# Kernel optimization log

Measured on AMD Instinct MI355X. Metric: run time of the kernel, lower is better.

The kernel has to match this reference:

```python
import jax, jax.numpy as jnp
import numpy as np

B, T, C, H = 4, 2048, 1024, 16
HD = C // H  # head dim = 64


def _rope(x, pos):
    """Rotary embedding. x: [B,H,T,hd], pos: [B,T] int positions."""
    half = x.shape[-1] // 2
    inv_freq = 1.0 / (10000.0 ** (jnp.arange(half, dtype=jnp.float32) / half))
    ang = pos.astype(jnp.float32)[:, None, :, None] * inv_freq  # [B,1,T,half]
    cos, sin = jnp.cos(ang), jnp.sin(ang)
    x1, x2 = x[..., :half], x[..., half:]
    return jnp.concatenate([x1 * cos - x2 * sin, x1 * sin + x2 * cos], axis=-1)


def setup_inputs() -> dict:
    key = jax.random.key(0)
    k1, k2, k3 = jax.random.split(key, 3)
    x = jax.random.normal(k1, (B, T, C), dtype=jnp.float32)
    W_attn = jax.random.normal(k2, (C, 3 * C), dtype=jnp.float32) * (1.0 / np.sqrt(C))
    W_proj = jax.random.normal(k3, (C, C), dtype=jnp.float32) * (1.0 / np.sqrt(C))
    indices = jnp.broadcast_to(jnp.arange(T, dtype=jnp.int32)[None, :], (B, T))
    return {"x": x, "W_attn": W_attn, "W_proj": W_proj, "indices": indices}


def reference(x, W_attn, W_proj, indices):
    # QKV projection (bias=False)
    qkv = x @ W_attn  # [B,T,3C]
    q, k, v = jnp.split(qkv, 3, axis=-1)

    def to_heads(t):
        return t.reshape(B, T, H, HD).transpose(0, 2, 1, 3)  # [B,H,T,hd]

    q, k, v = to_heads(q), to_heads(k), to_heads(v)
    # RoPE on q and k at positions given by indices (pos_emb_closure.adapt_*)
    q = _rope(q, indices)
    k = _rope(k, indices)

    # attn_mask = k_indices <= q_indices, shape [B,1,T,T]
    mask = indices[:, None, None, :] <= indices[:, None, :, None]

    att = jnp.einsum("bhqd,bhkd->bhqk", q, k) * (1.0 / np.sqrt(HD))
    att = jnp.where(mask, att, jnp.float32(-jnp.inf))
    att = jax.nn.softmax(att, axis=-1)
    y = jnp.einsum("bhqk,bhkd->bhqd", att, v)  # [B,H,T,hd]
    y = y.transpose(0, 2, 1, 3).reshape(B, T, C)
    return y @ W_proj
```

## Files before the change

### kernel.cpp

```cpp
#include <hip/hip_runtime.h>
#include <math.h>

namespace {
constexpr int Bsz = 4;
constexpr int T   = 2048;
constexpr int C   = 1024;
constexpr int H   = 16;
constexpr int HD  = 64;

typedef short bf16x8 __attribute__((ext_vector_type(8)));
typedef float f32x4  __attribute__((ext_vector_type(4)));
typedef unsigned int u32x4 __attribute__((ext_vector_type(4)));

#if defined(__has_builtin)
#if __has_builtin(__builtin_amdgcn_global_load_lds)
#define HAVE_GLL 1
typedef __attribute__((address_space(3))) unsigned int lds_u32_t;
typedef __attribute__((address_space(1))) unsigned int g_u32_t;
#define GLL16(gp, lp)                                                        \
  __builtin_amdgcn_global_load_lds((const g_u32_t*)(gp), (lds_u32_t*)(lp),   \
                                   16, 0, 0)
#endif
#endif

__device__ __forceinline__ unsigned short f2bf(float f) {
  unsigned int u = __builtin_bit_cast(unsigned int, f);
  u += 0x7FFFu + ((u >> 16) & 1u);
  return (unsigned short)(u >> 16);
}
__device__ __forceinline__ float bf2f(unsigned short s) {
  unsigned int u = ((unsigned int)s) << 16;
  return __builtin_bit_cast(float, u);
}
__device__ __forceinline__ unsigned int cvtpk_bf16(float a, float b) {
  unsigned int r;
  asm("v_cvt_pk_bf16_f32 %0, %1, %2" : "=v"(r) : "v"(a), "v"(b));
  return r;
}

__global__ __launch_bounds__(256) void f32_to_bf16_kernel(
    const float* __restrict__ in, unsigned short* __restrict__ out, int n4) {
  int i = blockIdx.x * 256 + threadIdx.x;
  if (i < n4) {
    float4 v = ((const float4*)in)[i];
    ushort4 o;
    o.x = f2bf(v.x); o.y = f2bf(v.y); o.z = f2bf(v.z); o.w = f2bf(v.w);
    ((ushort4*)out)[i] = o;
  }
}

__global__ __launch_bounds__(256) void transpose_bf16_kernel(
    const float* __restrict__ W, unsigned short* __restrict__ Wt, int K, int N) {
  __shared__ float tile[32][33];
  const int n0 = blockIdx.x * 32, k0 = blockIdx.y * 32;
  const int r = threadIdx.x >> 3, c4 = threadIdx.x & 7;
  float4 v = *(const float4*)(W + (size_t)(k0 + r) * N + n0 + c4 * 4);
  tile[r][c4 * 4 + 0] = v.x;
  tile[r][c4 * 4 + 1] = v.y;
  tile[r][c4 * 4 + 2] = v.z;
  tile[r][c4 * 4 + 3] = v.w;
  __syncthreads();
  ushort4 o;
  o.x = f2bf(tile[c4 * 4 + 0][r]);
  o.y = f2bf(tile[c4 * 4 + 1][r]);
  o.z = f2bf(tile[c4 * 4 + 2][r]);
  o.w = f2bf(tile[c4 * 4 + 3][r]);
  *(ushort4*)(Wt + (size_t)(n0 + r) * K + k0 + c4 * 4) = o;
}

template <int MODE>
__global__ __launch_bounds__(256) void gemm_bt(
    const unsigned short* __restrict__ A, const unsigned short* __restrict__ Bt,
    float* __restrict__ Cout, unsigned short* __restrict__ qp,
    unsigned short* __restrict__ kp, unsigned short* __restrict__ vp,
    int M, int N, int K) {
  __shared__ __align__(16) unsigned short As[128 * 32];
  __shared__ __align__(16) unsigned short Bs[128 * 32];
  const int tid = threadIdx.x;
  const int lane = tid & 63, w = tid >> 6;
  const int wr = w & 1, wc = w >> 1;
  const int l15 = lane & 15, quad = lane >> 4;
  const int m0 = blockIdx.y * 128, n0 = blockIdx.x * 128;

  const int srow = lane >> 2;
  const int schunk = (lane & 3) * 8;
  const unsigned short* gA = A + (size_t)(m0 + w * 32 + srow) * K + schunk;
  const unsigned short* gB = Bt + (size_t)(n0 + w * 32 + srow) * K + schunk;
  unsigned short* lA0 = &As[(w * 32) * 32 + lane * 8];
  unsigned short* lA1 = &As[(w * 32 + 16) * 32 + lane * 8];
  unsigned short* lB0 = &Bs[(w * 32) * 32 + lane * 8];
  unsigned short* lB1 = &Bs[(w * 32 + 16) * 32 + lane * 8];

  f32x4 acc[4][4] = {};

  for (int k0 = 0; k0 < K; k0 += 32) {
    __syncthreads();
#ifdef HAVE_GLL
    GLL16(gA + k0, lA0);
    GLL16(gA + (size_t)16 * K + k0, lA1);
    GLL16(gB + k0, lB0);
    GLL16(gB + (size_t)16 * K + k0, lB1);
#else
    *(uint4*)lA0 = *(const uint4*)(gA + k0);
    *(uint4*)lA1 = *(const uint4*)(gA + (size_t)16 * K + k0);
    *(uint4*)lB0 = *(const uint4*)(gB + k0);
    *(uint4*)lB1 = *(const uint4*)(gB + (size_t)16 * K + k0);
#endif
    __syncthreads();

    bf16x8 af[4], bfr[4];
#pragma unroll
    for (int mf = 0; mf < 4; ++mf)
      af[mf] = *(const bf16x8*)&As[(wr * 64 + mf * 16 + l15) * 32 + quad * 8];
#pragma unroll
    for (int nf = 0; nf < 4; ++nf)
      bfr[nf] = *(const bf16x8*)&Bs[(wc * 64 + nf * 16 + l15) * 32 + quad * 8];
#pragma unroll
    for (int mf = 0; mf < 4; ++mf)
#pragma unroll
      for (int nf = 0; nf < 4; ++nf)
        acc[mf][nf] = __builtin_amdgcn_mfma_f32_16x16x32_bf16(
            af[mf], bfr[nf], acc[mf][nf], 0, 0, 0);
  }

#pragma unroll
  for (int mf = 0; mf < 4; ++mf) {
    const int row0 = m0 + wr * 64 + mf * 16 + quad * 4;
#pragma unroll
    for (int nf = 0; nf < 4; ++nf) {
      if (MODE == 0) {
#pragma unroll
        for (int r = 0; r < 4; ++r) {
          const int col = n0 + wc * 64 + nf * 16 + l15;
          Cout[(size_t)(row0 + r) * N + col] = acc[mf][nf][r];
        }
      } else {
        const int col = n0 + wc * 64 + nf * 16 + l15;
        const int which = col >> 10;
        const int rem = col & (C - 1);
        const int h = rem >> 6, hd = rem & 63;
        const int b = row0 >> 11, t0 = row0 & (T - 1);
        if (which == 2) {
          ushort4 pv;
          pv.x = f2bf(acc[mf][nf][0]);
          pv.y = f2bf(acc[mf][nf][1]);
          pv.z = f2bf(acc[mf][nf][2]);
          pv.w = f2bf(acc[mf][nf][3]);
          *(ushort4*)(vp + (((size_t)(b * H + h)) * HD + hd) * T + t0) = pv;
        } else {
          unsigned short* dst = which == 0 ? qp : kp;
#pragma unroll
          for (int r = 0; r < 4; ++r)
            dst[(((size_t)(b * H + h)) * T + t0 + r) * HD + hd] =
                f2bf(acc[mf][nf][r]);
        }
      }
    }
  }
}

__global__ __launch_bounds__(256) void rope_bf16(unsigned short* __restrict__ q,
                                                 unsigned short* __restrict__ k,
                                                 const int* __restrict__ idx) {
  const int g = blockIdx.x * 8 + (threadIdx.x >> 5);
  const int lane = threadIdx.x & 31;
  const int b = g >> 11, t = g & (T - 1);
  const int pos = idx[b * T + t];
  const float inv = exp2f((float)lane * -0.41524101186f);
  float sn, cs;
  sincosf((float)pos * inv, &sn, &cs);
  const float SC = 0.18033688f;
  const float snq = sn * SC, csq = cs * SC;
  const size_t base0 = ((size_t)b * H * T + t) * HD + lane;
#pragma unroll 4
  for (int h = 0; h < H; ++h) {
    const size_t base = base0 + (size_t)h * T * HD;
    float x1 = bf2f(q[base]), x2 = bf2f(q[base + 32]);
    q[base]      = f2bf(x1 * csq - x2 * snq);
    q[base + 32] = f2bf(x1 * snq + x2 * csq);
    x1 = bf2f(k[base]);
    x2 = bf2f(k[base + 32]);
    k[base]      = f2bf(x1 * cs - x2 * sn);
    k[base + 32] = f2bf(x1 * sn + x2 * cs);
  }
}

__global__ __launch_bounds__(256) void flash_attn_mfma(
    const unsigned short* __restrict__ q, const unsigned short* __restrict__ k,
    const unsigned short* __restrict__ vt, const int* __restrict__ idx,
    unsigned short* __restrict__ y) {
  __shared__ __align__(16) unsigned short Ks[2][64 * 64];
  __shared__ __align__(16) unsigned short Vts[2][64 * 64];

  const int tid = threadIdx.x;
  const int lane = tid & 63, w = tid >> 6;
  const int l15 = lane & 15, quad = lane >> 4;

  const int flat = (blockIdx.z * H + blockIdx.y) * 16 + blockIdx.x;
  const int slot_ = flat >> 3;
  const int bh_i = (flat & 7) * 8 + (slot_ >> 4);
  const int bx = slot_ & 15;
  const int h = bh_i & (H - 1), b = bh_i >> 4;

  const size_t bh = (size_t)bh_i;
  const unsigned short* qg = q + bh * T * HD;
  const unsigned short* kg = k + bh * T * HD;
  const unsigned short* vg = vt + bh * HD * T;
  const int* idxb = idx + b * T;

  int km;
  {
    const int4* p4 = (const int4*)(idxb + (lane << 5));
    int4 v0 = p4[0];
    int m = max(max(v0.x, v0.y), max(v0.z, v0.w));
#pragma unroll
    for (int j = 1; j < 8; ++j) {
      int4 v = p4[j];
      m = max(m, max(max(v.x, v.y), max(v.z, v.w)));
    }
    km = max(m, __shfl_xor(m, 1));
  }

  const int r1 = tid >> 3, c1 = tid & 7;
  const int r2 = r1 + 32;
  const int xr1 = (r1 & 7) << 3;
  const int swS1 = r1 * 64 + ((c1 * 8) ^ xr1);
  const int swS2 = r2 * 64 + ((c1 * 8) ^ xr1);
  const int vbase = 32 * (c1 >> 2) + 16 * (c1 & 1) + 4 * ((c1 >> 1) & 1);
  const int vo1a = r1 * 64 + ((vbase + 0) ^ xr1);
  const int vo1b = r1 * 64 + ((vbase + 8) ^ xr1);
  const int vo2a = r2 * 64 + ((vbase + 0) ^ xr1);
  const int vo2b = r2 * 64 + ((vbase + 8) ^ xr1);
  const int rx = (l15 & 7) << 3;

  for (int ti = 0; ti < 2; ++ti) {
    const int qt = (ti == 0) ? bx : 31 - bx;
    const int qrow = qt * 64 + w * 16 + l15;

    const bf16x8 bq0 = *(const bf16x8*)(qg + (size_t)qrow * HD + quad * 8);
    const bf16x8 bq1 = *(const bf16x8*)(qg + (size_t)qrow * HD + 32 + quad * 8);
    const int pq = idxb[qrow];
    int mq = pq;
    mq = min(mq, __shfl_xor(mq, 1));
    mq = min(mq, __shfl_xor(mq, 2));
    mq = min(mq, __shfl_xor(mq, 4));
    mq = min(mq, __shfl_xor(mq, 8));
    const unsigned long long bal = __ballot(km > mq);

    float m_run = -1e38f, lq = 0.0f;
    f32x4 Oa[4] = {};

    {
      uint4 ka = *(const uint4*)(kg + (size_t)r1 * HD + c1 * 8);
      uint4 kb = *(const uint4*)(kg + (size_t)r2 * HD + c1 * 8);
      uint4 va = *(const uint4*)(vg + (size_t)r1 * T + c1 * 8);
      uint4 vb = *(const uint4*)(vg + (size_t)r2 * T + c1 * 8);
      __syncthreads();
      *(uint4*)&Ks[0][swS1] = ka;
      *(uint4*)&Ks[0][swS2] = kb;
      *(uint2*)&Vts[0][vo1a] = make_uint2(va.x, va.y);
      *(uint2*)&Vts[0][vo1b] = make_uint2(va.z, va.w);
      *(uint2*)&Vts[0][vo2a] = make_uint2(vb.x, vb.y);
      *(uint2*)&Vts[0][vo2b] = make_uint2(vb.z, vb.w);
    }

    for (int kt = 0; kt <= qt; ++kt) {
      const int cur = kt & 1;
      const int k0 = kt * 64;
      __syncthreads();

      uint4 nka, nkb, nva, nvb;
      if (kt < qt) {
        const int kn = k0 + 64;
        nka = *(const uint4*)(kg + (size_t)(kn + r1) * HD + c1 * 8);
        nkb = *(const uint4*)(kg + (size_t)(kn + r2) * HD + c1 * 8);
        nva = *(const uint4*)(vg + (size_t)r1 * T + kn + c1 * 8);
        nvb = *(const uint4*)(vg + (size_t)r2 * T + kn + c1 * 8);
      }

      f32x4 Sa[4];
      __builtin_amdgcn_s_setprio(1);
#pragma unroll
      for (int nf = 0; nf < 4; ++nf) {
        const int row = (nf * 16 + l15) * 64;
        bf16x8 ak0 = *(const bf16x8*)&Ks[cur][row + ((quad * 8) ^ rx)];
        bf16x8 ak1 = *(const bf16x8*)&Ks[cur][row + ((32 + quad * 8) ^ rx)];
        f32x4 s = {};
        s = __builtin_amdgcn_mfma_f32_16x16x32_bf16(ak0, bq0, s, 0, 0, 0);
        s = __builtin_amdgcn_mfma_f32_16x16x32_bf16(ak1, bq1, s, 0, 0, 0);
        Sa[nf] = s;
      }
      __builtin_amdgcn_s_setprio(0);

      if ((bal >> (kt + kt)) & 1ull) {
#pragma unroll
        for (int nf = 0; nf < 4; ++nf) {
          const int4 pk4 = *(const int4*)(idxb + k0 + nf * 16 + quad * 4);
          if (pk4.x > pq) Sa[nf][0] = -3e38f;
          if (pk4.y > pq) Sa[nf][1] = -3e38f;
          if (pk4.z > pq) Sa[nf][2] = -3e38f;
          if (pk4.w > pq) Sa[nf][3] = -3e38f;
        }
      }

      float mx = fmaxf(
          fmaxf(fmaxf(fmaxf(Sa[0][0], Sa[0][1]), Sa[0][2]),
                fmaxf(fmaxf(Sa[0][3], Sa[1][0]), Sa[1][1])),
          fmaxf(fmaxf(fmaxf(Sa[1][2], Sa[1][3]), Sa[2][0]),
                fmaxf(fmaxf(Sa[2][1], Sa[2][2]), Sa[2][3])));
      mx = fmaxf(mx, fmaxf(fmaxf(Sa[3][0], Sa[3][1]), fmaxf(Sa[3][2], Sa[3][3])));
      mx = fmaxf(mx, __shfl_xor(mx, 16));
      mx = fmaxf(mx, __shfl_xor(mx, 32));

      if (!__all(mx <= m_run + 8.0f)) {
        const float mn = fmaxf(m_run, mx);
        const float alpha = exp2f(m_run - mn);
        m_run = mn;
        lq *= alpha;
#pragma unroll
        for (int nfd = 0; nfd < 4; ++nfd)
#pragma unroll
          for (int r = 0; r < 4; ++r) Oa[nfd][r] *= alpha;
      }

      u32x4 w0, w1;
#pragma unroll
      for (int nf = 0; nf < 4; ++nf) {
        float p0 = exp2f(Sa[nf][0] - m_run);
        float p1 = exp2f(Sa[nf][1] - m_run);
        float p2 = exp2f(Sa[nf][2] - m_run);
        float p3 = exp2f(Sa[nf][3] - m_run);
        Sa[nf][0] = p0; Sa[nf][1] = p1; Sa[nf][2] = p2; Sa[nf][3] = p3;
        if (nf < 2) {
          w0[nf * 2 + 0] = cvtpk_bf16(p0, p1);
          w0[nf * 2 + 1] = cvtpk_bf16(p2, p3);
        } else {
          w1[(nf - 2) * 2 + 0] = cvtpk_bf16(p0, p1);
          w1[(nf - 2) * 2 + 1] = cvtpk_bf16(p2, p3);
        }
      }
      const bf16x8 bp0 = __builtin_bit_cast(bf16x8, w0);
      const bf16x8 bp1 = __builtin_bit_cast(bf16x8, w1);

      __builtin_amdgcn_s_setprio(1);
#pragma unroll
      for (int nfd = 0; nfd < 4; ++nfd) {
        const int vrow = (nfd * 16 + l15) * 64;
        bf16x8 av0 = *(const bf16x8*)&Vts[cur][vrow + ((quad * 8) ^ rx)];
        bf16x8 av1 = *(const bf16x8*)&Vts[cur][vrow + ((32 + quad * 8) ^ rx)];
        Oa[nfd] = __builtin_amdgcn_mfma_f32_16x16x32_bf16(av0, bp0, Oa[nfd], 0, 0, 0);
        Oa[nfd] = __builtin_amdgcn_mfma_f32_16x16x32_bf16(av1, bp1, Oa[nfd], 0, 0, 0);
      }
      __builtin_amdgcn_s_setprio(0);

      lq += ((Sa[0][0] + Sa[0][1]) + (Sa[0][2] + Sa[0][3])) +
            ((Sa[1][0] + Sa[1][1]) + (Sa[1][2] + Sa[1][3])) +
            ((Sa[2][0] + Sa[2][1]) + (Sa[2][2] + Sa[2][3])) +
            ((Sa[3][0] + Sa[3][1]) + (Sa[3][2] + Sa[3][3]));

      if (kt < qt) {
        const int nxt = cur ^ 1;
        *(uint4*)&Ks[nxt][swS1] = nka;
        *(uint4*)&Ks[nxt][swS2] = nkb;
        *(uint2*)&Vts[nxt][vo1a] = make_uint2(nva.x, nva.y);
        *(uint2*)&Vts[nxt][vo1b] = make_uint2(nva.z, nva.w);
        *(uint2*)&Vts[nxt][vo2a] = make_uint2(nvb.x, nvb.y);
        *(uint2*)&Vts[nxt][vo2b] = make_uint2(nvb.z, nvb.w);
      }
    }

    float lsum = lq;
    lsum += __shfl_xor(lsum, 16);
    lsum += __shfl_xor(lsum, 32);
    const float rl = 1.0f / lsum;
    const size_t base = ((size_t)b * T + qrow) * (size_t)C + h * HD;
#pragma unroll
    for (int nfd = 0; nfd < 4; ++nfd) {
      ushort4 o;
      o.x = f2bf(Oa[nfd][0] * rl);
      o.y = f2bf(Oa[nfd][1] * rl);
      o.z = f2bf(Oa[nfd][2] * rl);
      o.w = f2bf(Oa[nfd][3] * rl);
      *(ushort4*)(y + base + nfd * 16 + quad * 4) = o;
    }
  }
}

}

extern "C" void kernel_launch(void* const* d_in, const int* in_sizes, int n_in,
                              void* d_out, int out_size, void* d_ws,
                              size_t ws_size, hipStream_t stream) {
  const float* x      = (const float*)d_in[0];
  const float* W_attn = (const float*)d_in[1];
  const float* W_proj = (const float*)d_in[2];
  const int* indices  = (const int*)d_in[3];
  float* out = (float*)d_out;

  const size_t nM = (size_t)Bsz * T * C;
  unsigned short* xb  = (unsigned short*)d_ws;
  unsigned short* wat = xb + nM;
  unsigned short* wpt = wat + (size_t)3 * C * C;
  unsigned short* qp  = wpt + (size_t)C * C;
  unsigned short* kp  = qp + nM;
  unsigned short* vp  = kp + nM;
  unsigned short* yb  = vp + nM;

  f32_to_bf16_kernel<<<(int)(nM / 4 / 256), 256, 0, stream>>>(x, xb, (int)(nM / 4));
  transpose_bf16_kernel<<<dim3(3 * C / 32, C / 32), 256, 0, stream>>>(W_attn, wat, C, 3 * C);
  transpose_bf16_kernel<<<dim3(C / 32, C / 32), 256, 0, stream>>>(W_proj, wpt, C, C);
  gemm_bt<1><<<dim3(3 * C / 128, Bsz * T / 128), 256, 0, stream>>>(
      xb, wat, nullptr, qp, kp, vp, Bsz * T, 3 * C, C);
  rope_bf16<<<(Bsz * T) / 8, 256, 0, stream>>>(qp, kp, indices);
  flash_attn_mfma<<<dim3(16, H, Bsz), 256, 0, stream>>>(qp, kp, vp, indices, yb);
  gemm_bt<0><<<dim3(C / 128, Bsz * T / 128), 256, 0, stream>>>(
      yb, wpt, out, nullptr, nullptr, nullptr, Bsz * T, C, C);
}
```

Before: 304.5 us.

## Fuse RoPE into QKV GEMM epilogue and give each attention block one query tile

```diff
diff --git a/kernel.cpp b/kernel.cpp
--- a/kernel.cpp
+++ b/kernel.cpp
@@ -73,7 +73,7 @@
     const unsigned short* __restrict__ A, const unsigned short* __restrict__ Bt,
     float* __restrict__ Cout, unsigned short* __restrict__ qp,
     unsigned short* __restrict__ kp, unsigned short* __restrict__ vp,
-    int M, int N, int K) {
+    const int* __restrict__ idx, int M, int N, int K) {
   __shared__ __align__(16) unsigned short As[128 * 32];
   __shared__ __align__(16) unsigned short Bs[128 * 32];
   const int tid = threadIdx.x;
@@ -123,65 +123,66 @@
             af[mf], bfr[nf], acc[mf][nf], 0, 0, 0);
   }
 
-#pragma unroll
-  for (int mf = 0; mf < 4; ++mf) {
-    const int row0 = m0 + wr * 64 + mf * 16 + quad * 4;
-#pragma unroll
-    for (int nf = 0; nf < 4; ++nf) {
-      if (MODE == 0) {
-#pragma unroll
-        for (int r = 0; r < 4; ++r) {
-          const int col = n0 + wc * 64 + nf * 16 + l15;
+  if (MODE == 0) {
+#pragma unroll
+    for (int mf = 0; mf < 4; ++mf) {
+      const int row0 = m0 + wr * 64 + mf * 16 + quad * 4;
+#pragma unroll
+      for (int nf = 0; nf < 4; ++nf) {
+        const int col = n0 + wc * 64 + nf * 16 + l15;
+#pragma unroll
+        for (int r = 0; r < 4; ++r)
           Cout[(size_t)(row0 + r) * N + col] = acc[mf][nf][r];
-        }
-      } else {
-        const int col = n0 + wc * 64 + nf * 16 + l15;
-        const int which = col >> 10;
-        const int rem = col & (C - 1);
-        const int h = rem >> 6, hd = rem & 63;
+      }
+    }
+  } else {
+    const int colbase = n0 + wc * 64;
+    const int which = colbase >> 10;
+    if (which == 2) {
+#pragma unroll
+      for (int mf = 0; mf < 4; ++mf) {
+        const int row0 = m0 + wr * 64 + mf * 16 + quad * 4;
         const int b = row0 >> 11, t0 = row0 & (T - 1);
-        if (which == 2) {
+#pragma unroll
+        for (int nf = 0; nf < 4; ++nf) {
+          const int rem = (colbase + nf * 16 + l15) & (C - 1);
+          const int h = rem >> 6, hd = rem & 63;
           ushort4 pv;
           pv.x = f2bf(acc[mf][nf][0]);
           pv.y = f2bf(acc[mf][nf][1]);
           pv.z = f2bf(acc[mf][nf][2]);
           pv.w = f2bf(acc[mf][nf][3]);
           *(ushort4*)(vp + (((size_t)(b * H + h)) * HD + hd) * T + t0) = pv;
-        } else {
-          unsigned short* dst = which == 0 ? qp : kp;
-#pragma unroll
-          for (int r = 0; r < 4; ++r)
-            dst[(((size_t)(b * H + h)) * T + t0 + r) * HD + hd] =
-                f2bf(acc[mf][nf][r]);
         }
       }
-    }
-  }
-}
-
-__global__ __launch_bounds__(256) void rope_bf16(unsigned short* __restrict__ q,
-                                                 unsigned short* __restrict__ k,
-                                                 const int* __restrict__ idx) {
-  const int g = blockIdx.x * 8 + (threadIdx.x >> 5);
-  const int lane = threadIdx.x & 31;
-  const int b = g >> 11, t = g & (T - 1);
-  const int pos = idx[b * T + t];
-  const float inv = exp2f((float)lane * -0.41524101186f);
-  float sn, cs;
-  sincosf((float)pos * inv, &sn, &cs);
-  const float SC = 0.18033688f;
-  const float snq = sn * SC, csq = cs * SC;
-  const size_t base0 = ((size_t)b * H * T + t) * HD + lane;
-#pragma unroll 4
-  for (int h = 0; h < H; ++h) {
-    const size_t base = base0 + (size_t)h * T * HD;
-    float x1 = bf2f(q[base]), x2 = bf2f(q[base + 32]);
-    q[base]      = f2bf(x1 * csq - x2 * snq);
-    q[base + 32] = f2bf(x1 * snq + x2 * csq);
-    x1 = bf2f(k[base]);
-    x2 = bf2f(k[base + 32]);
-    k[base]      = f2bf(x1 * cs - x2 * sn);
-    k[base + 32] = f2bf(x1 * sn + x2 * cs);
+    } else {
+      unsigned short* dst = (which == 0) ? qp : kp;
+      const float sc = (which == 0) ? 0.18033688f : 1.0f;
+      const int h = ((colbase + l15) & (C - 1)) >> 6;
+      const float inv0 = exp2f((float)l15 * -0.41524101186f);
+      const float inv1 = exp2f((float)(16 + l15) * -0.41524101186f);
+#pragma unroll
+      for (int mf = 0; mf < 4; ++mf) {
+        const int row0 = m0 + wr * 64 + mf * 16 + quad * 4;
+        const int b = row0 >> 11, t0 = row0 & (T - 1);
+        const int4 pos4 = *(const int4*)(idx + b * T + t0);
+        const int pr[4] = {pos4.x, pos4.y, pos4.z, pos4.w};
+        const size_t obase = ((size_t)(b * H + h)) * T + t0;
+#pragma unroll
+        for (int nf = 0; nf < 2; ++nf) {
+          const float inv = (nf == 0) ? inv0 : inv1;
+          const int d = nf * 16 + l15;
+#pragma unroll
+          for (int r = 0; r < 4; ++r) {
+            float sn, cs;
+            sincosf((float)pr[r] * inv, &sn, &cs);
+            const float x1 = acc[mf][nf][r], x2 = acc[mf][nf + 2][r];
+            dst[(obase + r) * HD + d]      = f2bf((x1 * cs - x2 * sn) * sc);
+            dst[(obase + r) * HD + d + 32] = f2bf((x1 * sn + x2 * cs) * sc);
+          }
+        }
+      }
+    }
   }
 }
 
@@ -196,10 +197,10 @@
   const int lane = tid & 63, w = tid >> 6;
   const int l15 = lane & 15, quad = lane >> 4;
 
-  const int flat = (blockIdx.z * H + blockIdx.y) * 16 + blockIdx.x;
-  const int slot_ = flat >> 3;
-  const int bh_i = (flat & 7) * 8 + (slot_ >> 4);
-  const int bx = slot_ & 15;
+  const int flat = (blockIdx.z * H + blockIdx.y) * 32 + blockIdx.x;
+  const int slot = flat >> 3;
+  const int bh_i = (flat & 7) * 8 + (slot >> 5);
+  const int qt = 31 - (slot & 31);
   const int h = bh_i & (H - 1), b = bh_i >> 4;
 
   const size_t bh = (size_t)bh_i;
@@ -233,156 +234,152 @@
   const int vo2b = r2 * 64 + ((vbase + 8) ^ xr1);
   const int rx = (l15 & 7) << 3;
 
-  for (int ti = 0; ti < 2; ++ti) {
-    const int qt = (ti == 0) ? bx : 31 - bx;
-    const int qrow = qt * 64 + w * 16 + l15;
-
-    const bf16x8 bq0 = *(const bf16x8*)(qg + (size_t)qrow * HD + quad * 8);
-    const bf16x8 bq1 = *(const bf16x8*)(qg + (size_t)qrow * HD + 32 + quad * 8);
-    const int pq = idxb[qrow];
-    int mq = pq;
-    mq = min(mq, __shfl_xor(mq, 1));
-    mq = min(mq, __shfl_xor(mq, 2));
-    mq = min(mq, __shfl_xor(mq, 4));
-    mq = min(mq, __shfl_xor(mq, 8));
-    const unsigned long long bal = __ballot(km > mq);
-
-    float m_run = -1e38f, lq = 0.0f;
-    f32x4 Oa[4] = {};
-
-    {
-      uint4 ka = *(const uint4*)(kg + (size_t)r1 * HD + c1 * 8);
-      uint4 kb = *(const uint4*)(kg + (size_t)r2 * HD + c1 * 8);
-      uint4 va = *(const uint4*)(vg + (size_t)r1 * T + c1 * 8);
-      uint4 vb = *(const uint4*)(vg + (size_t)r2 * T + c1 * 8);
-      __syncthreads();
-      *(uint4*)&Ks[0][swS1] = ka;
-      *(uint4*)&Ks[0][swS2] = kb;
-      *(uint2*)&Vts[0][vo1a] = make_uint2(va.x, va.y);
-      *(uint2*)&Vts[0][vo1b] = make_uint2(va.z, va.w);
-      *(uint2*)&Vts[0][vo2a] = make_uint2(vb.x, vb.y);
-      *(uint2*)&Vts[0][vo2b] = make_uint2(vb.z, vb.w);
-    }
-
-    for (int kt = 0; kt <= qt; ++kt) {
-      const int cur = kt & 1;
-      const int k0 = kt * 64;
-      __syncthreads();
-
-      uint4 nka, nkb, nva, nvb;
-      if (kt < qt) {
-        const int kn = k0 + 64;
-        nka = *(const uint4*)(kg + (size_t)(kn + r1) * HD + c1 * 8);
-        nkb = *(const uint4*)(kg + (size_t)(kn + r2) * HD + c1 * 8);
-        nva = *(const uint4*)(vg + (size_t)r1 * T + kn + c1 * 8);
-        nvb = *(const uint4*)(vg + (size_t)r2 * T + kn + c1 * 8);
+  const int qrow = qt * 64 + w * 16 + l15;
+
+  const bf16x8 bq0 = *(const bf16x8*)(qg + (size_t)qrow * HD + quad * 8);
+  const bf16x8 bq1 = *(const bf16x8*)(qg + (size_t)qrow * HD + 32 + quad * 8);
+  const int pq = idxb[qrow];
+  int mq = pq;
+  mq = min(mq, __shfl_xor(mq, 1));
+  mq = min(mq, __shfl_xor(mq, 2));
+  mq = min(mq, __shfl_xor(mq, 4));
+  mq = min(mq, __shfl_xor(mq, 8));
+  const unsigned long long bal = __ballot(km > mq);
+
+  float m_run = -1e38f, lq = 0.0f;
+  f32x4 Oa[4] = {};
+
+  {
+    uint4 ka = *(const uint4*)(kg + (size_t)r1 * HD + c1 * 8);
+    uint4 kb = *(const uint4*)(kg + (size_t)r2 * HD + c1 * 8);
+    uint4 va = *(const uint4*)(vg + (size_t)r1 * T + c1 * 8);
+    uint4 vb = *(const uint4*)(vg + (size_t)r2 * T + c1 * 8);
+    *(uint4*)&Ks[0][swS1] = ka;
+    *(uint4*)&Ks[0][swS2] = kb;
+    *(uint2*)&Vts[0][vo1a] = make_uint2(va.x, va.y);
+    *(uint2*)&Vts[0][vo1b] = make_uint2(va.z, va.w);
+    *(uint2*)&Vts[0][vo2a] = make_uint2(vb.x, vb.y);
+    *(uint2*)&Vts[0][vo2b] = make_uint2(vb.z, vb.w);
+  }
+
+  for (int kt = 0; kt <= qt; ++kt) {
+    const int cur = kt & 1;
+    const int k0 = kt * 64;
+    __syncthreads();
+
+    uint4 nka, nkb, nva, nvb;
+    if (kt < qt) {
+      const int kn = k0 + 64;
+      nka = *(const uint4*)(kg + (size_t)(kn + r1) * HD + c1 * 8);
+      nkb = *(const uint4*)(kg + (size_t)(kn + r2) * HD + c1 * 8);
+      nva = *(const uint4*)(vg + (size_t)r1 * T + kn + c1 * 8);
+      nvb = *(const uint4*)(vg + (size_t)r2 * T + kn + c1 * 8);
+    }
+
+    f32x4 Sa[4];
+    __builtin_amdgcn_s_setprio(1);
+#pragma unroll
+    for (int nf = 0; nf < 4; ++nf) {
+      const int row = (nf * 16 + l15) * 64;
+      bf16x8 ak0 = *(const bf16x8*)&Ks[cur][row + ((quad * 8) ^ rx)];
+      bf16x8 ak1 = *(const bf16x8*)&Ks[cur][row + ((32 + quad * 8) ^ rx)];
+      f32x4 s = {};
+      s = __builtin_amdgcn_mfma_f32_16x16x32_bf16(ak0, bq0, s, 0, 0, 0);
+      s = __builtin_amdgcn_mfma_f32_16x16x32_bf16(ak1, bq1, s, 0, 0, 0);
+      Sa[nf] = s;
+    }
+    __builtin_amdgcn_s_setprio(0);
+
+    if ((bal >> (kt + kt)) & 1ull) {
+#pragma unroll
+      for (int nf = 0; nf < 4; ++nf) {
+        const int4 pk4 = *(const int4*)(idxb + k0 + nf * 16 + quad * 4);
+        if (pk4.x > pq) Sa[nf][0] = -3e38f;
+        if (pk4.y > pq) Sa[nf][1] = -3e38f;
+        if (pk4.z > pq) Sa[nf][2] = -3e38f;
+        if (pk4.w > pq) Sa[nf][3] = -3e38f;
       }
-
-      f32x4 Sa[4];
-      __builtin_amdgcn_s_setprio(1);
-#pragma unroll
-      for (int nf = 0; nf < 4; ++nf) {
-        const int row = (nf * 16 + l15) * 64;
-        bf16x8 ak0 = *(const bf16x8*)&Ks[cur][row + ((quad * 8) ^ rx)];
-        bf16x8 ak1 = *(const bf16x8*)&Ks[cur][row + ((32 + quad * 8) ^ rx)];
-        f32x4 s = {};
-        s = __builtin_amdgcn_mfma_f32_16x16x32_bf16(ak0, bq0, s, 0, 0, 0);
-        s = __builtin_amdgcn_mfma_f32_16x16x32_bf16(ak1, bq1, s, 0, 0, 0);
-        Sa[nf] = s;
+    }
+
+    float mx = fmaxf(
+        fmaxf(fmaxf(fmaxf(Sa[0][0], Sa[0][1]), Sa[0][2]),
+              fmaxf(fmaxf(Sa[0][3], Sa[1][0]), Sa[1][1])),
+        fmaxf(fmaxf(fmaxf(Sa[1][2], Sa[1][3]), Sa[2][0]),
+              fmaxf(fmaxf(Sa[2][1], Sa[2][2]), Sa[2][3])));
+    mx = fmaxf(mx, fmaxf(fmaxf(Sa[3][0], Sa[3][1]), fmaxf(Sa[3][2], Sa[3][3])));
+    mx = fmaxf(mx, __shfl_xor(mx, 16));
+    mx = fmaxf(mx, __shfl_xor(mx, 32));
+
+    if (!__all(mx <= m_run + 8.0f)) {
+      const float mn = fmaxf(m_run, mx);
+      const float alpha = exp2f(m_run - mn);
+      m_run = mn;
+      lq *= alpha;
+#pragma unroll
+      for (int nfd = 0; nfd < 4; ++nfd)
+#pragma unroll
+        for (int r = 0; r < 4; ++r) Oa[nfd][r] *= alpha;
+    }
+
+    u32x4 w0, w1;
+#pragma unroll
+    for (int nf = 0; nf < 4; ++nf) {
+      float p0 = exp2f(Sa[nf][0] - m_run);
+      float p1 = exp2f(Sa[nf][1] - m_run);
+      float p2 = exp2f(Sa[nf][2] - m_run);
+      float p3 = exp2f(Sa[nf][3] - m_run);
+      Sa[nf][0] = p0; Sa[nf][1] = p1; Sa[nf][2] = p2; Sa[nf][3] = p3;
+      if (nf < 2) {
+        w0[nf * 2 + 0] = cvtpk_bf16(p0, p1);
+        w0[nf * 2 + 1] = cvtpk_bf16(p2, p3);
+      } else {
+        w1[(nf - 2) * 2 + 0] = cvtpk_bf16(p0, p1);
+        w1[(nf - 2) * 2 + 1] = cvtpk_bf16(p2, p3);
       }
-      __builtin_amdgcn_s_setprio(0);
-
-      if ((bal >> (kt + kt)) & 1ull) {
-#pragma unroll
-        for (int nf = 0; nf < 4; ++nf) {
-          const int4 pk4 = *(const int4*)(idxb + k0 + nf * 16 + quad * 4);
-          if (pk4.x > pq) Sa[nf][0] = -3e38f;
-          if (pk4.y > pq) Sa[nf][1] = -3e38f;
-          if (pk4.z > pq) Sa[nf][2] = -3e38f;
-          if (pk4.w > pq) Sa[nf][3] = -3e38f;
-        }
-      }
-
-      float mx = fmaxf(
-          fmaxf(fmaxf(fmaxf(Sa[0][0], Sa[0][1]), Sa[0][2]),
-                fmaxf(fmaxf(Sa[0][3], Sa[1][0]), Sa[1][1])),
-          fmaxf(fmaxf(fmaxf(Sa[1][2], Sa[1][3]), Sa[2][0]),
-                fmaxf(fmaxf(Sa[2][1], Sa[2][2]), Sa[2][3])));
-      mx = fmaxf(mx, fmaxf(fmaxf(Sa[3][0], Sa[3][1]), fmaxf(Sa[3][2], Sa[3][3])));
-      mx = fmaxf(mx, __shfl_xor(mx, 16));
-      mx = fmaxf(mx, __shfl_xor(mx, 32));
-
-      if (!__all(mx <= m_run + 8.0f)) {
-        const float mn = fmaxf(m_run, mx);
-        const float alpha = exp2f(m_run - mn);
-        m_run = mn;
-        lq *= alpha;
-#pragma unroll
-        for (int nfd = 0; nfd < 4; ++nfd)
-#pragma unroll
-          for (int r = 0; r < 4; ++r) Oa[nfd][r] *= alpha;
-      }
-
-      u32x4 w0, w1;
-#pragma unroll
-      for (int nf = 0; nf < 4; ++nf) {
-        float p0 = exp2f(Sa[nf][0] - m_run);
-        float p1 = exp2f(Sa[nf][1] - m_run);
-        float p2 = exp2f(Sa[nf][2] - m_run);
-        float p3 = exp2f(Sa[nf][3] - m_run);
-        Sa[nf][0] = p0; Sa[nf][1] = p1; Sa[nf][2] = p2; Sa[nf][3] = p3;
-        if (nf < 2) {
-          w0[nf * 2 + 0] = cvtpk_bf16(p0, p1);
-          w0[nf * 2 + 1] = cvtpk_bf16(p2, p3);
-        } else {
-          w1[(nf - 2) * 2 + 0] = cvtpk_bf16(p0, p1);
-          w1[(nf - 2) * 2 + 1] = cvtpk_bf16(p2, p3);
-        }
-      }
-      const bf16x8 bp0 = __builtin_bit_cast(bf16x8, w0);
-      const bf16x8 bp1 = __builtin_bit_cast(bf16x8, w1);
-
-      __builtin_amdgcn_s_setprio(1);
-#pragma unroll
-      for (int nfd = 0; nfd < 4; ++nfd) {
-        const int vrow = (nfd * 16 + l15) * 64;
-        bf16x8 av0 = *(const bf16x8*)&Vts[cur][vrow + ((quad * 8) ^ rx)];
-        bf16x8 av1 = *(const bf16x8*)&Vts[cur][vrow + ((32 + quad * 8) ^ rx)];
-        Oa[nfd] = __builtin_amdgcn_mfma_f32_16x16x32_bf16(av0, bp0, Oa[nfd], 0, 0, 0);
-        Oa[nfd] = __builtin_amdgcn_mfma_f32_16x16x32_bf16(av1, bp1, Oa[nfd], 0, 0, 0);
-      }
-      __builtin_amdgcn_s_setprio(0);
-
-      lq += ((Sa[0][0] + Sa[0][1]) + (Sa[0][2] + Sa[0][3])) +
-            ((Sa[1][0] + Sa[1][1]) + (Sa[1][2] + Sa[1][3])) +
-            ((Sa[2][0] + Sa[2][1]) + (Sa[2][2] + Sa[2][3])) +
-            ((Sa[3][0] + Sa[3][1]) + (Sa[3][2] + Sa[3][3]));
-
-      if (kt < qt) {
-        const int nxt = cur ^ 1;
-        *(uint4*)&Ks[nxt][swS1] = nka;
-        *(uint4*)&Ks[nxt][swS2] = nkb;
-        *(uint2*)&Vts[nxt][vo1a] = make_uint2(nva.x, nva.y);
-        *(uint2*)&Vts[nxt][vo1b] = make_uint2(nva.z, nva.w);
-        *(uint2*)&Vts[nxt][vo2a] = make_uint2(nvb.x, nvb.y);
-        *(uint2*)&Vts[nxt][vo2b] = make_uint2(nvb.z, nvb.w);
-      }
-    }
-
-    float lsum = lq;
-    lsum += __shfl_xor(lsum, 16);
-    lsum += __shfl_xor(lsum, 32);
-    const float rl = 1.0f / lsum;
-    const size_t base = ((size_t)b * T + qrow) * (size_t)C + h * HD;
+    }
+    const bf16x8 bp0 = __builtin_bit_cast(bf16x8, w0);
+    const bf16x8 bp1 = __builtin_bit_cast(bf16x8, w1);
+
+    __builtin_amdgcn_s_setprio(1);
 #pragma unroll
     for (int nfd = 0; nfd < 4; ++nfd) {
-      ushort4 o;
-      o.x = f2bf(Oa[nfd][0] * rl);
-      o.y = f2bf(Oa[nfd][1] * rl);
-      o.z = f2bf(Oa[nfd][2] * rl);
-      o.w = f2bf(Oa[nfd][3] * rl);
-      *(ushort4*)(y + base + nfd * 16 + quad * 4) = o;
-    }
+      const int vrow = (nfd * 16 + l15) * 64;
+      bf16x8 av0 = *(const bf16x8*)&Vts[cur][vrow + ((quad * 8) ^ rx)];
+      bf16x8 av1 = *(const bf16x8*)&Vts[cur][vrow + ((32 + quad * 8) ^ rx)];
+      Oa[nfd] = __builtin_amdgcn_mfma_f32_16x16x32_bf16(av0, bp0, Oa[nfd], 0, 0, 0);
+      Oa[nfd] = __builtin_amdgcn_mfma_f32_16x16x32_bf16(av1, bp1, Oa[nfd], 0, 0, 0);
+    }
+    __builtin_amdgcn_s_setprio(0);
+
+    lq += ((Sa[0][0] + Sa[0][1]) + (Sa[0][2] + Sa[0][3])) +
+          ((Sa[1][0] + Sa[1][1]) + (Sa[1][2] + Sa[1][3])) +
+          ((Sa[2][0] + Sa[2][1]) + (Sa[2][2] + Sa[2][3])) +
+          ((Sa[3][0] + Sa[3][1]) + (Sa[3][2] + Sa[3][3]));
+
+    if (kt < qt) {
+      const int nxt = cur ^ 1;
+      *(uint4*)&Ks[nxt][swS1] = nka;
+      *(uint4*)&Ks[nxt][swS2] = nkb;
+      *(uint2*)&Vts[nxt][vo1a] = make_uint2(nva.x, nva.y);
+      *(uint2*)&Vts[nxt][vo1b] = make_uint2(nva.z, nva.w);
+      *(uint2*)&Vts[nxt][vo2a] = make_uint2(nvb.x, nvb.y);
+      *(uint2*)&Vts[nxt][vo2b] = make_uint2(nvb.z, nvb.w);
+    }
+  }
+
+  float lsum = lq;
+  lsum += __shfl_xor(lsum, 16);
+  lsum += __shfl_xor(lsum, 32);
+  const float rl = 1.0f / lsum;
+  const size_t base = ((size_t)b * T + qrow) * (size_t)C + h * HD;
+#pragma unroll
+  for (int nfd = 0; nfd < 4; ++nfd) {
+    ushort4 o;
+    o.x = f2bf(Oa[nfd][0] * rl);
+    o.y = f2bf(Oa[nfd][1] * rl);
+    o.z = f2bf(Oa[nfd][2] * rl);
+    o.w = f2bf(Oa[nfd][3] * rl);
+    *(ushort4*)(y + base + nfd * 16 + quad * 4) = o;
   }
 }
 
@@ -410,9 +407,8 @@
   transpose_bf16_kernel<<<dim3(3 * C / 32, C / 32), 256, 0, stream>>>(W_attn, wat, C, 3 * C);
   transpose_bf16_kernel<<<dim3(C / 32, C / 32), 256, 0, stream>>>(W_proj, wpt, C, C);
   gemm_bt<1><<<dim3(3 * C / 128, Bsz * T / 128), 256, 0, stream>>>(
-      xb, wat, nullptr, qp, kp, vp, Bsz * T, 3 * C, C);
-  rope_bf16<<<(Bsz * T) / 8, 256, 0, stream>>>(qp, kp, indices);
-  flash_attn_mfma<<<dim3(16, H, Bsz), 256, 0, stream>>>(qp, kp, vp, indices, yb);
+      xb, wat, nullptr, qp, kp, vp, indices, Bsz * T, 3 * C, C);
+  flash_attn_mfma<<<dim3(32, H, Bsz), 256, 0, stream>>>(qp, kp, vp, indices, yb);
   gemm_bt<0><<<dim3(C / 128, Bsz * T / 128), 256, 0, stream>>>(
-      yb, wpt, out, nullptr, nullptr, nullptr, Bsz * T, C, C);
-}
+      yb, wpt, out, nullptr, nullptr, nullptr, nullptr, Bsz * T, C, C);
+}
```

Measured after the change: 299.8 us. No clear change (-1.5%).
